# Optimization experiments

Measured on AMD Instinct MI355X. Metric: run time of the kernel, lower is better.

Reference implementation:

```python
import math
from collections import deque
import jax, jax.numpy as jnp
import numpy as np

PS = 16; DF = 256; DS = 16; DLANG = 896; BETA = 2.0
B_SZ = 2; IMG = 512


def setup_inputs():
    key = jax.random.key(0)
    ks = jax.random.split(key, 16)
    def rn(k, shape, scale=1.0):
        return jax.random.normal(k, shape, jnp.float32) * scale
    # W_delta bias init: inverse-softplus of dt ~ LogUniform(1e-3, 1e-1), as in torch _init_weights
    u = jax.random.uniform(ks[15], (DF,), jnp.float32)
    dt = jnp.exp(u * (math.log(0.1) - math.log(0.001)) + math.log(0.001))
    inv_dt = dt + jnp.log(-jnp.expm1(-dt))
    return {
        "images": rn(ks[0], (B_SZ, 3, IMG, IMG)),
        "lang_g": rn(ks[1], (B_SZ, DLANG)),
        "conv1_w": rn(ks[2], (64, 3, 3, 3), 1.0 / math.sqrt(27)),
        "conv1_b": jnp.zeros((64,), jnp.float32),
        "conv2_w": rn(ks[3], (128, 64, 3, 3), 1.0 / math.sqrt(576)),
        "conv2_b": jnp.zeros((128,), jnp.float32),
        "fc_w": rn(ks[4], (DF, 128), 1.0 / math.sqrt(128)),
        "fc_b": jnp.zeros((DF,), jnp.float32),
        "W_gate": rn(ks[5], (DF, DLANG), 1.0 / math.sqrt(DLANG)),
        "W_g_prime": rn(ks[6], (DF, DLANG), 1.0 / math.sqrt(DLANG)),
        "A_log": jnp.log(jnp.broadcast_to(jnp.arange(1, DS + 1, dtype=jnp.float32), (DF, DS))),
        "D": jnp.ones((DF,), jnp.float32),
        "B_w": rn(ks[7], (DS, DF), 1.0 / math.sqrt(DF)),
        "B_b": jnp.zeros((DS,), jnp.float32),
        "C_w": rn(ks[8], (DS, DF), 1.0 / math.sqrt(DF)),
        "C_b": jnp.zeros((DS,), jnp.float32),
        "Wd_w": rn(ks[9], (DF, DF), 1.0 / math.sqrt(DF)),
        "Wd_b": inv_dt,
        "out_w": rn(ks[10], (DF, DF), 1.0 / math.sqrt(DF)),
        "out_b": jnp.zeros((DF,), jnp.float32),
        "ln_g": jnp.ones((DF,), jnp.float32),
        "ln_b": jnp.zeros((DF,), jnp.float32),
    }


def _gelu(x):
    return jax.nn.gelu(x, approximate=False)  # torch nn.GELU() default = exact erf


def _conv(x, w, b):
    y = jax.lax.conv_general_dilated(x, w, (1, 1), 'SAME', dimension_numbers=('NCHW', 'OIHW', 'NCHW'))
    return y + b[None, :, None, None]


def _patch_feats(images, c1w, c1b, c2w, c2b, fcw, fcb):
    B, C, H, W = images.shape
    nH, nW = H // PS, W // PS
    # non-overlapping patchify (== unfold/unfold in torch)
    p = images.reshape(B, C, nH, PS, nW, PS).transpose(0, 2, 4, 1, 3, 5).reshape(B * nH * nW, C, PS, PS)
    h = _gelu(_conv(p, c1w, c1b))
    h = _gelu(_conv(h, c2w, c2b))
    h = h.mean(axis=(2, 3))  # AdaptiveAvgPool2d((1,1))
    feats = (h @ fcw.T + fcb).reshape(B, nH * nW, DF)
    return feats, nH, nW


def _structure(feats, r_sem, nH, nW):
    # Host-side (numpy) Kruskal MST + BFS ordering, mirroring the torch detach().cpu() path.
    f = np.asarray(feats, np.float32)
    r = np.asarray(r_sem, np.float32)
    B, P, _ = f.shape
    src, dst = [], []
    for i in range(nH):
        for j in range(nW):
            u = i * nW + j
            if j + 1 < nW:
                src.append(u); dst.append(u + 1)
            if i + 1 < nH:
                src.append(u); dst.append(u + nW)
    src = np.array(src); dst = np.array(dst)
    bfs_all, par_all = [], []
    for b in range(B):
        fn = f[b] / np.maximum(np.linalg.norm(f[b], axis=1, keepdims=True), 1e-12)
        cos = (fn[src] * fn[dst]).sum(1)
        w = (1.0 - r[b][src]) * (1.0 - r[b][dst]) * (-cos) + 1e-6
        parent = np.arange(P)
        def find(x):
            while parent[x] != x:
                parent[x] = parent[parent[x]]
                x = parent[x]
            return x
        adj = [[] for _ in range(P)]
        cnt = 0
        for idx in np.argsort(w):
            ru, rv = find(int(src[idx])), find(int(dst[idx]))
            if ru != rv:
                parent[ru] = rv
                adj[src[idx]].append(int(dst[idx]))
                adj[dst[idx]].append(int(src[idx]))
                cnt += 1
                if cnt == P - 1:
                    break
        root = int(r[b].argmax())
        vis = [False] * P; par_of = [-1] * P; bfs = []
        q = deque([root]); vis[root] = True
        while q:
            n = q.popleft()
            bfs.append(n)
            for nb in adj[n]:
                if not vis[nb]:
                    vis[nb] = True
                    par_of[nb] = n
                    q.append(nb)
        o2b = [0] * P
        for bi, oi in enumerate(bfs):
            o2b[oi] = bi
        par_bfs = [-1 if par_of[o] == -1 else o2b[par_of[o]] for o in bfs]
        bfs_all.append(bfs); par_all.append(par_bfs)
    return jnp.array(bfs_all, jnp.int32), jnp.array(par_all, jnp.int32)


def _core(feats, r_sem, g_prime, bfs, par, A_log, D, B_w, B_b, C_w, C_b, Wd_w, Wd_b, out_w, out_b, ln_g, ln_b):
    A = -jnp.exp(A_log)  # (DF, DS)
    def one(f_b, r_b, gp, bfs_b, par_b):
        rs = r_b[bfs_b]                                  # (P,)
        X = f_b[bfs_b] + rs[:, None] * gp[None, :]       # (P, DF)
        delta = jax.nn.softplus(X @ Wd_w.T + Wd_b) * (1.0 + BETA * rs[:, None])
        Bp = X @ B_w.T + B_b                             # (P, DS)
        Cp = X @ C_w.T + C_b                             # (P, DS)
        P = X.shape[0]
        def body(H, inp):
            i, d_i, b_i, c_i, x_i, p_i = inp
            A_bar = jnp.exp(d_i[:, None] * A)            # (DF, DS)
            h_par = H[jnp.maximum(p_i, 0)] * (p_i >= 0)  # zeros at root
            h = A_bar * h_par + (d_i[:, None] * b_i[None, :]) * x_i[:, None]
            H = H.at[i].set(h)
            y = (h * c_i[None, :]).sum(-1) + D * x_i
            return H, y
        H0 = jnp.zeros((P, DF, DS), X.dtype)
        _, Y = jax.lax.scan(body, H0, (jnp.arange(P), delta, Bp, Cp, X, par_b))
        Yr = jnp.zeros_like(Y).at[bfs_b].set(Y)          # scatter back to raster order
        o = Yr @ out_w.T + out_b
        mu = o.mean(-1, keepdims=True)
        v = ((o - mu) ** 2).mean(-1, keepdims=True)
        return ln_g * (o - mu) / jnp.sqrt(v + 1e-5) + ln_b
    return jax.vmap(one)(feats, r_sem, g_prime, bfs, par)


def reference(images, lang_g, conv1_w, conv1_b, conv2_w, conv2_b, fc_w, fc_b, W_gate, W_g_prime, A_log, D, B_w, B_b, C_w, C_b, Wd_w, Wd_b, out_w, out_b, ln_g, ln_b):
    feats, nH, nW = _patch_feats(images, conv1_w, conv1_b, conv2_w, conv2_b, fc_w, fc_b)
    g_proj = lang_g @ W_gate.T
    r_sem = jax.nn.sigmoid(jnp.einsum('bd,bpd->bp', g_proj, feats) / math.sqrt(DF))
    bfs, par = _structure(feats, r_sem, nH, nW)
    g_prime = lang_g @ W_g_prime.T
    return _core(feats, r_sem, g_prime, bfs, par, A_log, D, B_w, B_b, C_w, C_b, Wd_w, Wd_b, out_w, out_b, ln_g, ln_b)
```

## Files before the change

kernel.cpp:

```cpp
#include <hip/hip_runtime.h>
#include <cstddef>
#include <cstdint>

#define NB    2
#define NP    1024
#define DFEAT 256
#define DSTATE 16
#define NEDGE 1984

typedef unsigned short ushortb;

typedef float fx16 __attribute__((ext_vector_type(16)));
typedef short s16x8 __attribute__((ext_vector_type(8)));

__device__ __forceinline__ float bf2f(unsigned short u){
  union { unsigned int i; float f; } c; c.i = ((unsigned int)u) << 16; return c.f;
}
__device__ __forceinline__ unsigned short f2bf(float f){
  union { float f; unsigned int i; } c; c.f = f;
  unsigned int u = c.i;
  unsigned int r = (u + 0x7fffu + ((u >> 16) & 1u)) >> 16;
  return (unsigned short)r;
}
__device__ __forceinline__ float ldin(const void* p, size_t i, int isbf){
  return isbf ? bf2f(((const ushortb*)p)[i]) : ((const float*)p)[i];
}
__device__ __forceinline__ float gelu_f(float x){
  return 0.5f * x * (1.0f + erff(x * 0.70710678118654752f));
}
__device__ __forceinline__ unsigned int f2sort(float f){
  union { float f; unsigned int i; } c; c.f = f;
  return (c.i & 0x80000000u) ? ~c.i : (c.i | 0x80000000u);
}

constexpr size_t AL(size_t x){ return (x + 63) & ~(size_t)63; }
constexpr size_t O_W1    = 0;
constexpr size_t O_B1    = AL(O_W1 + 1728);
constexpr size_t O_W2    = AL(O_B1 + 64);
constexpr size_t O_B2    = AL(O_W2 + 73728);
constexpr size_t O_FCW   = AL(O_B2 + 128);
constexpr size_t O_FCB   = AL(O_FCW + 32768);
constexpr size_t O_WDW   = AL(O_FCB + 256);
constexpr size_t O_WDB   = AL(O_WDW + 65536);
constexpr size_t O_BWO   = AL(O_WDB + 256);
constexpr size_t O_BBO   = AL(O_BWO + 4096);
constexpr size_t O_CWO   = AL(O_BBO + 16);
constexpr size_t O_CBO   = AL(O_CWO + 4096);
constexpr size_t O_OW    = AL(O_CBO + 16);
constexpr size_t O_OB    = AL(O_OW + 65536);
constexpr size_t O_AF    = AL(O_OB + 256);
constexpr size_t O_DD    = AL(O_AF + 4096);
constexpr size_t O_LNG   = AL(O_DD + 256);
constexpr size_t O_LNB   = AL(O_LNG + 256);
constexpr size_t O_FEATS = AL(O_LNB + 256);
constexpr size_t O_GPROJ = AL(O_FEATS + (size_t)NB*NP*DFEAT);
constexpr size_t O_GPRIM = AL(O_GPROJ + NB*DFEAT);
constexpr size_t O_RSEM  = AL(O_GPRIM + NB*DFEAT);
constexpr size_t O_BFS   = AL(O_RSEM + NB*NP);
constexpr size_t O_PAR   = AL(O_BFS + NB*NP);
constexpr size_t O_X     = AL(O_PAR + NB*NP);
constexpr size_t O_DELTA = AL(O_X + (size_t)NB*NP*DFEAT);
constexpr size_t O_BP    = AL(O_DELTA + (size_t)NB*NP*DFEAT);
constexpr size_t O_CP    = AL(O_BP + NB*NP*DSTATE);
constexpr size_t O_YR    = AL(O_CP + NB*NP*DSTATE);
constexpr size_t O_FLAG  = AL(O_YR + (size_t)NB*NP*DFEAT);
constexpr size_t O_LVL   = AL(O_FLAG + 64);

__global__ __launch_bounds__(256) void k_sniff(const void* img, float* ws)
{
  __shared__ int cnt;
  int tid = threadIdx.x;
  if (tid == 0) cnt = 0;
  __syncthreads();
  const ushortb* u = (const ushortb*)img;
  int local = 0;
  for (int k = 0; k < 16; k++){
    unsigned short v = u[tid * 16 + k];
    if (v == 0 || v == 0x8000u){ local++; continue; }
    float f = fabsf(bf2f(v));
    if (f >= 1e-8f && f <= 64.f) local++;
  }
  atomicAdd(&cnt, local);
  __syncthreads();
  if (tid == 0) ((int*)(ws + O_FLAG))[0] = (cnt >= 3900) ? 1 : 0;
}

__global__ __launch_bounds__(256) void k_convert(const void* c1w, const void* c1b, const void* c2w,
                          const void* c2b, const void* fcw, const void* fcb,
                          const void* alog, const void* dvec,
                          const void* bw, const void* bb, const void* cw, const void* cb,
                          const void* wdw, const void* wdb,
                          const void* ow, const void* ob,
                          const void* lng, const void* lnb,
                          const void* lang, const void* wgate, const void* wgp,
                          float* ws)
{
  const int F = ((const int*)(ws + O_FLAG))[0];
  if (blockIdx.x >= 3038){
    int row = (blockIdx.x - 3038) * 4 + (threadIdx.x >> 6);
    int lane = threadIdx.x & 63;
    int mat = row >> 9;
    int b   = (row >> 8) & 1;
    int df  = row & 255;
    const void* W = mat ? wgp : wgate;
    float s = 0.f;
    for (int k = lane; k < 896; k += 64)
      s += ldin(lang, (size_t)b * 896 + k, F) * ldin(W, (size_t)df * 896 + k, F);
    s += __shfl_xor(s, 1);  s += __shfl_xor(s, 2);  s += __shfl_xor(s, 4);
    s += __shfl_xor(s, 8);  s += __shfl_xor(s, 16); s += __shfl_xor(s, 32);
    if (lane == 0) ws[(mat ? O_GPRIM : O_GPROJ) + b * 256 + df] = s;
    return;
  }
  if (blockIdx.x >= 990){
    size_t i2 = (size_t)(blockIdx.x - 990) * 256 + threadIdx.x;
    if (i2 < (size_t)NB * NP * DFEAT) ws[O_YR + i2] = 0.f;
    return;
  }
  int i = blockIdx.x * 256 + threadIdx.x;
  if (i < 1728){ ws[O_W1 + i] = ldin(c1w, i, F); return; } i -= 1728;
  if (i < 64){ ws[O_B1 + i] = ldin(c1b, i, F); return; } i -= 64;
  if (i < 73728){
    int s = i >> 11;
    int r = i & 2047;
    int nt = r >> 9;
    int r2 = r & 511;
    int ln = r2 >> 3, e = r2 & 7;
    int oc = nt * 32 + (ln & 31);
    int k  = s * 16 + (ln >> 5) * 8 + e;
    int ic = k & 63, tap = k >> 6;
    float v = ldin(c2w, (size_t)(oc * 64 + ic) * 9 + tap, F);
    ushortb hi = f2bf(v);
    float lo = v - bf2f(hi);
    ushortb* WB = (ushortb*)(ws + O_W2);
    size_t cb = ((size_t)(s * 4 + nt)) * 2;
    WB[cb * 512 + r2]       = hi;
    WB[(cb + 1) * 512 + r2] = f2bf(lo);
    return;
  } i -= 73728;
  if (i < 128){ ws[O_B2 + i] = ldin(c2b, i, F); return; } i -= 128;
  if (i < 32768){ ws[O_FCW + i] = ldin(fcw, i, F); return; } i -= 32768;
  if (i < 256){ ws[O_FCB + i] = ldin(fcb, i, F); return; } i -= 256;
  if (i < 65536){
    int k = i >> 8, df = i & 255;
    ws[O_WDW + i] = ldin(wdw, (size_t)df * 256 + k, F); return;
  } i -= 65536;
  if (i < 256){ ws[O_WDB + i] = ldin(wdb, i, F); return; } i -= 256;
  if (i < 4096){
    int k = i >> 4, s = i & 15;
    ws[O_BWO + i] = ldin(bw, (size_t)s * 256 + k, F); return;
  } i -= 4096;
  if (i < 16){ ws[O_BBO + i] = ldin(bb, i, F); return; } i -= 16;
  if (i < 4096){
    int k = i >> 4, s = i & 15;
    ws[O_CWO + i] = ldin(cw, (size_t)s * 256 + k, F); return;
  } i -= 4096;
  if (i < 16){ ws[O_CBO + i] = ldin(cb, i, F); return; } i -= 16;
  if (i < 65536){
    int k = i >> 8, df = i & 255;
    ws[O_OW + i] = ldin(ow, (size_t)df * 256 + k, F); return;
  } i -= 65536;
  if (i < 256){ ws[O_OB + i] = ldin(ob, i, F); return; } i -= 256;
  if (i < 4096){ ws[O_AF + i] = -expf(ldin(alog, i, F)); return; } i -= 4096;
  if (i < 256){ ws[O_DD + i] = ldin(dvec, i, F); return; } i -= 256;
  if (i < 256){ ws[O_LNG + i] = ldin(lng, i, F); return; } i -= 256;
  if (i < 256){ ws[O_LNB + i] = ldin(lnb, i, F); }
}

__global__ __launch_bounds__(512, 2) void k_patch(const void* __restrict__ img,
                                                  const float* __restrict__ ws,
                                                  float* __restrict__ feats)
{
  __shared__ __align__(16) ushortb Ahi[18 * 18 * 64];
  __shared__ __align__(16) ushortb Alo[18 * 18 * 64];
  __shared__ float timg[768];
  __shared__ float pool4[512];
  __shared__ float pm[128];
  const int F = ((const int*)(ws + O_FLAG))[0];
  const float* W1 = ws + O_W1;  const float* B1 = ws + O_B1;
  const float* FCW = ws + O_FCW; const float* FCB = ws + O_FCB;
  const s16x8* BF = (const s16x8*)(ws + O_W2);

  int blk = blockIdx.x; int b = blk >> 10; int pidx = blk & 1023;
  int ph = pidx >> 5, pw = pidx & 31;
  int tid = threadIdx.x;

  if (tid < 256){
    int y = tid >> 4, x = tid & 15;
    #pragma unroll
    for (int c = 0; c < 3; c++)
      timg[c * 256 + tid] =
        ldin(img, (((size_t)b * 3 + c) * 512 + (ph * 16 + y)) * 512 + (pw * 16 + x), F);
  }
  {
    uint4 z4 = make_uint4(0u, 0u, 0u, 0u);
    for (int r = tid; r < 324; r += 512){
      int y = r / 18, x = r - y * 18;
      if (y == 0 || y == 17 || x == 0 || x == 17){
        #pragma unroll
        for (int m = 0; m < 8; m++){
          *(uint4*)&Ahi[r * 64 + m * 8] = z4;
          *(uint4*)&Alo[r * 64 + m * 8] = z4;
        }
      }
    }
  }
  __syncthreads();

  {
    int p = tid & 255, og = tid >> 8;
    int ii = p >> 4, jj = p & 15;
    float pin[27];
    #pragma unroll
    for (int c = 0; c < 3; c++)
      #pragma unroll
      for (int dy = 0; dy < 3; dy++)
        #pragma unroll
        for (int dx = 0; dx < 3; dx++){
          int y = ii + dy - 1, x = jj + dx - 1;
          bool ok = (y >= 0 && y < 16 && x >= 0 && x < 16);
          pin[c * 9 + dy * 3 + dx] = ok ? timg[c * 256 + y * 16 + x] : 0.f;
        }
    int w1base = __builtin_amdgcn_readfirstlane(og * 32 * 27);
    const float* W1g = W1 + w1base;
    float av[32];
    #pragma unroll
    for (int o = 0; o < 32; o++){
      int oc = og * 32 + o;
      float a = B1[oc];
      #pragma unroll
      for (int t = 0; t < 27; t++) a += W1g[o * 27 + t] * pin[t];
      av[o] = gelu_f(a);
    }
    int r = (ii + 1) * 18 + (jj + 1);
    int sw = (r & 7) << 3;
    #pragma unroll
    for (int m = 0; m < 4; m++){
      unsigned int hp[4], lp[4];
      #pragma unroll
      for (int q = 0; q < 4; q++){
        float v0 = av[m * 8 + 2 * q], v1 = av[m * 8 + 2 * q + 1];
        ushortb h0 = f2bf(v0), h1 = f2bf(v1);
        float l0 = v0 - bf2f(h0), l1 = v1 - bf2f(h1);
        hp[q] = (unsigned int)h0 | ((unsigned int)h1 << 16);
        lp[q] = (unsigned int)f2bf(l0) | ((unsigned int)f2bf(l1) << 16);
      }
      int idx = r * 64 + ((og * 32 + m * 8) ^ sw);
      *(uint4*)&Ahi[idx] = make_uint4(hp[0], hp[1], hp[2], hp[3]);
      *(uint4*)&Alo[idx] = make_uint4(lp[0], lp[1], lp[2], lp[3]);
    }
  }
  __syncthreads();

  int wv = tid >> 6, ln = tid & 63;
  int mg = wv >> 1, ng = wv & 1;
  int l31 = ln & 31, lhi = ln >> 5;
  int xcol = ln & 15, yrow = l31 >> 4;

  fx16 acc[2][2];
  #pragma unroll
  for (int m = 0; m < 2; m++)
    #pragma unroll
    for (int n = 0; n < 2; n++)
      #pragma unroll
      for (int r = 0; r < 16; r++) acc[m][n][r] = 0.f;

#define LDFRAG(S, FA, FB) { \
    int sl = (S); if (sl > 35) sl = 35; \
    int shf = sl >> 2, sub = sl & 3; \
    int dyq = shf / 3, dxq = shf - dyq * 3; \
    int ic0 = sub * 16 + lhi * 8; \
    { int r_ = (mg * 4 + yrow + dyq) * 18 + xcol + dxq; \
      int idx = r_ * 64 + (ic0 ^ ((r_ & 7) << 3)); \
      FA[0][0] = *(const s16x8*)&Ahi[idx]; \
      FA[0][1] = *(const s16x8*)&Alo[idx]; } \
    { int r_ = (mg * 4 + 2 + yrow + dyq) * 18 + xcol + dxq; \
      int idx = r_ * 64 + (ic0 ^ ((r_ & 7) << 3)); \
      FA[1][0] = *(const s16x8*)&Ahi[idx]; \
      FA[1][1] = *(const s16x8*)&Alo[idx]; } \
    { int cb = (sl * 4 + ng * 2) * 2; \
      FB[0][0] = BF[cb * 64 + ln]; \
      FB[0][1] = BF[cb * 64 + 64 + ln]; \
      FB[1][0] = BF[cb * 64 + 128 + ln]; \
      FB[1][1] = BF[cb * 64 + 192 + ln]; } \
  }

#define MSTEP(FA, FB) { \
    acc[0][0] = __builtin_amdgcn_mfma_f32_32x32x16_bf16(FA[0][0], FB[0][0], acc[0][0], 0, 0, 0); \
    acc[0][1] = __builtin_amdgcn_mfma_f32_32x32x16_bf16(FA[0][0], FB[1][0], acc[0][1], 0, 0, 0); \
    acc[1][0] = __builtin_amdgcn_mfma_f32_32x32x16_bf16(FA[1][0], FB[0][0], acc[1][0], 0, 0, 0); \
    acc[1][1] = __builtin_amdgcn_mfma_f32_32x32x16_bf16(FA[1][0], FB[1][0], acc[1][1], 0, 0, 0); \
    acc[0][0] = __builtin_amdgcn_mfma_f32_32x32x16_bf16(FA[0][1], FB[0][0], acc[0][0], 0, 0, 0); \
    acc[0][1] = __builtin_amdgcn_mfma_f32_32x32x16_bf16(FA[0][1], FB[1][0], acc[0][1], 0, 0, 0); \
    acc[1][0] = __builtin_amdgcn_mfma_f32_32x32x16_bf16(FA[1][1], FB[0][0], acc[1][0], 0, 0, 0); \
    acc[1][1] = __builtin_amdgcn_mfma_f32_32x32x16_bf16(FA[1][1], FB[1][0], acc[1][1], 0, 0, 0); \
    acc[0][0] = __builtin_amdgcn_mfma_f32_32x32x16_bf16(FA[0][0], FB[0][1], acc[0][0], 0, 0, 0); \
    acc[0][1] = __builtin_amdgcn_mfma_f32_32x32x16_bf16(FA[0][0], FB[1][1], acc[0][1], 0, 0, 0); \
    acc[1][0] = __builtin_amdgcn_mfma_f32_32x32x16_bf16(FA[1][0], FB[0][1], acc[1][0], 0, 0, 0); \
    acc[1][1] = __builtin_amdgcn_mfma_f32_32x32x16_bf16(FA[1][0], FB[1][1], acc[1][1], 0, 0, 0); \
  }

  {
    s16x8 fa0[2][2], fb0[2][2], fa1[2][2], fb1[2][2];
    LDFRAG(0, fa0, fb0);
    for (int s2 = 0; s2 < 18; s2++){
      LDFRAG(2 * s2 + 1, fa1, fb1);
      MSTEP(fa0, fb0);
      LDFRAG(2 * s2 + 2, fa0, fb0);
      MSTEP(fa1, fb1);
    }
  }
#undef LDFRAG
#undef MSTEP

  #pragma unroll
  for (int n = 0; n < 2; n++){
    int nt = ng * 2 + n;
    float bz = ws[O_B2 + nt * 32 + l31];
    float sum = 0.f;
    #pragma unroll
    for (int m = 0; m < 2; m++)
      #pragma unroll
      for (int r = 0; r < 16; r++)
        sum += gelu_f(acc[m][n][r] + bz);
    sum += __shfl_xor(sum, 32);
    if (lhi == 0) pool4[mg * 128 + nt * 32 + l31] = sum;
  }
  __syncthreads();
  if (tid < 128){
    float sv = pool4[tid] + pool4[128 + tid] + pool4[256 + tid] + pool4[384 + tid];
    pm[tid] = sv * (1.f / 256.f);
  }
  __syncthreads();

  if (tid < 256){
    int df = tid;
    float s = FCB[df];
    const float* wrow = FCW + (size_t)df * 128;
    #pragma unroll
    for (int k = 0; k < 128; k += 4)
      s += wrow[k] * pm[k] + wrow[k + 1] * pm[k + 1]
         + wrow[k + 2] * pm[k + 2] + wrow[k + 3] * pm[k + 3];
    feats[((size_t)(b * 1024 + pidx)) * 256 + df] = s;
  }
}

__device__ __forceinline__ void edge_uv(int e, int& u, int& v){
  if (e < 1953){
    int i = e / 63; int k = e - i * 63;
    if (k < 62){ int j = k >> 1; u = i * 32 + j; v = (k & 1) ? u + 32 : u + 1; }
    else { u = i * 32 + 31; v = u + 32; }
  } else { u = 31 * 32 + (e - 1953); v = u + 1; }
}

__global__ __launch_bounds__(1024) void k_struct(float* __restrict__ ws)
{
  __shared__ float s_ninv[1024];
  __shared__ float s_w[NEDGE];
  __shared__ float s_r[1024];
  __shared__ int   s_comp[1024];
  __shared__ int   s_link[1024];
  __shared__ int   s_link2[1024];
  __shared__ unsigned long long s_best[1024];
  __shared__ unsigned char  s_mst[NEDGE];
  __shared__ unsigned short s_adj[1024 * 4];
  __shared__ unsigned char  s_deg[1024];
  __shared__ unsigned short s_bfs[1024];
  __shared__ short          s_parof[1024];
  __shared__ unsigned short s_o2b[1024];
  __shared__ unsigned short s_cur[1024];
  __shared__ unsigned short s_nxt[1024];
  __shared__ unsigned short s_off[1025];
  __shared__ unsigned short s_loff2[1026];
  __shared__ unsigned long long s_rootkey;
  __shared__ int s_ncomp, s_cursz, s_bfscnt, s_nextsz, s_nlvl;

  int b = blockIdx.x; int tid = threadIdx.x;
  const float* feats = ws + O_FEATS + (size_t)b * NP * DFEAT;

  {
    const float4* f4 = (const float4*)(feats + (size_t)tid * 256);
    const float4* g4 = (const float4*)(ws + O_GPROJ + b * 256);
    float d = 0.f, gdot = 0.f;
    for (int k = 0; k < 64; k++){
      float4 q = f4[k]; float4 g = g4[k];
      d += q.x*q.x + q.y*q.y + q.z*q.z + q.w*q.w;
      gdot += q.x*g.x + q.y*g.y + q.z*g.z + q.w*g.w;
    }
    s_ninv[tid] = 1.f / fmaxf(sqrtf(d), 1e-12f);
    float r = 1.f / (1.f + expf(-gdot * (1.f / 16.f)));
    s_r[tid] = r;
    ws[O_RSEM + b * NP + tid] = r;
    s_comp[tid] = tid;
    s_deg[tid] = 0;
    s_bfs[tid] = (unsigned short)tid;
    s_o2b[tid] = (unsigned short)tid;
    s_parof[tid] = -1;
  }
  for (int e = tid; e < NEDGE; e += 1024) s_mst[e] = 0;
  __syncthreads();

  for (int e = tid; e < NEDGE; e += 1024){
    int u, v; edge_uv(e, u, v);
    const float4* fu = (const float4*)(feats + (size_t)u * 256);
    const float4* fv = (const float4*)(feats + (size_t)v * 256);
    float d = 0.f;
    for (int k = 0; k < 64; k++){ float4 a = fu[k], c = fv[k]; d += a.x*c.x + a.y*c.y + a.z*c.z + a.w*c.w; }
    float cosv = d * s_ninv[u] * s_ninv[v];
    s_w[e] = (1.f - s_r[u]) * (1.f - s_r[v]) * (-cosv) + 1e-6f;
  }
  __syncthreads();

  for (int round = 0; round < 12; round++){
    s_best[tid] = ~0ull;
    __syncthreads();
    for (int e = tid; e < NEDGE; e += 1024){
      int u, v; edge_uv(e, u, v);
      int cu = s_comp[u], cv = s_comp[v];
      if (cu != cv){
        unsigned long long key = (((unsigned long long)f2sort(s_w[e])) << 32) | (unsigned int)e;
        atomicMin(&s_best[cu], key);
        atomicMin(&s_best[cv], key);
      }
    }
    __syncthreads();
    int l = tid;
    if (s_comp[tid] == tid && s_best[tid] != ~0ull){
      int e = (int)(s_best[tid] & 0xffffffffu);
      int u, v; edge_uv(e, u, v);
      s_mst[e] = 1;
      int cu = s_comp[u], cv = s_comp[v];
      l = (cu == tid) ? cv : cu;
    }
    s_link[tid] = l;
    __syncthreads();
    if (l != tid && s_link[l] == tid && tid < l) s_link[tid] = tid;
    __syncthreads();
    for (int it = 0; it < 10; it++){
      int x = s_link[tid]; s_link2[tid] = s_link[x];
      __syncthreads();
      s_link[tid] = s_link2[tid];
      __syncthreads();
    }
    s_comp[tid] = s_link[s_comp[tid]];
    if (tid == 0) s_ncomp = 0;
    __syncthreads();
    if (s_comp[tid] == tid) atomicAdd(&s_ncomp, 1);
    __syncthreads();
    if (s_ncomp == 1) break;
    __syncthreads();
  }
  __syncthreads();

  {
    int v = tid; int i = v >> 5, j = v & 31;
    float wloc[4]; int nloc[4]; int d = 0;
    if (j > 0){ int e = (i < 31) ? (i * 63 + 2 * (j - 1)) : (1953 + (j - 1));
      if (s_mst[e]){ wloc[d] = s_w[e]; nloc[d] = v - 1; d++; } }
    if (j < 31){ int e = (i < 31) ? (i * 63 + 2 * j) : (1953 + j);
      if (s_mst[e]){ wloc[d] = s_w[e]; nloc[d] = v + 1; d++; } }
    if (i > 0){ int e = (i - 1) * 63 + ((j < 31) ? (2 * j + 1) : 62);
      if (s_mst[e]){ wloc[d] = s_w[e]; nloc[d] = v - 32; d++; } }
    if (i < 31){ int e = i * 63 + ((j < 31) ? (2 * j + 1) : 62);
      if (s_mst[e]){ wloc[d] = s_w[e]; nloc[d] = v + 32; d++; } }
    for (int a = 1; a < d; a++){
      float wv = wloc[a]; int nv = nloc[a]; int c = a - 1;
      while (c >= 0 && wloc[c] > wv){ wloc[c+1] = wloc[c]; nloc[c+1] = nloc[c]; c--; }
      wloc[c+1] = wv; nloc[c+1] = nv;
    }
    s_deg[v] = (unsigned char)d;
    for (int a = 0; a < d; a++) s_adj[v * 4 + a] = (unsigned short)nloc[a];
  }
  if (tid == 0) s_rootkey = 0ull;
  __syncthreads();
  {
    unsigned long long key = (((unsigned long long)f2sort(s_r[tid])) << 32) | (unsigned int)(1023 - tid);
    atomicMax(&s_rootkey, key);
  }
  __syncthreads();
  int root = 1023 - (int)(s_rootkey & 0xffffffffu);

  if (tid == 0){
    s_bfs[0] = (unsigned short)root; s_o2b[root] = 0; s_parof[root] = -1;
    s_cur[0] = (unsigned short)root; s_cursz = 1; s_bfscnt = 1; s_nlvl = 0;
  }
  __syncthreads();
  for (int lev = 0; lev < 1024; lev++){
    int csz = s_cursz;
    if (csz <= 0) break;
    if (tid < 64){
      int runbase = 0;
      for (int t0 = 0; t0 < csz; t0 += 64){
        int t = t0 + tid;
        int cnt = 0;
        if (t < csz){
          int n = s_cur[t];
          cnt = (int)s_deg[n] - (s_parof[n] >= 0 ? 1 : 0);
        }
        int v = cnt;
        #pragma unroll
        for (int off = 1; off < 64; off <<= 1){
          int u2 = __shfl_up(v, off);
          if (tid >= off) v += u2;
        }
        if (t < csz) s_off[t] = (unsigned short)(runbase + v - cnt);
        runbase += __shfl(v, 63);
      }
      if (tid == 0){
        if (s_nlvl < 1025){ s_loff2[s_nlvl] = (unsigned short)(s_bfscnt - csz); }
        s_nlvl++;
        s_nextsz = runbase;
      }
    }
    __syncthreads();
    if (tid < csz){
      int n = s_cur[tid]; int base = s_off[tid]; int k = 0;
      int pn = s_parof[n]; int dg = s_deg[n];
      for (int a = 0; a < dg; a++){
        int c = s_adj[n * 4 + a];
        if (c == pn) continue;
        s_parof[c] = (short)n;
        if (base + k < 1024) s_nxt[base + k] = (unsigned short)c;
        int pos = s_bfscnt + base + k;
        if (pos < 1024){
          s_bfs[pos] = (unsigned short)c;
          s_o2b[c] = (unsigned short)pos;
        }
        k++;
      }
    }
    __syncthreads();
    if (tid == 0){ s_bfscnt += s_nextsz; s_cursz = (s_nextsz > 1024) ? 1024 : s_nextsz; }
    __syncthreads();
    if (tid < s_cursz) s_cur[tid] = s_nxt[tid];
    __syncthreads();
  }
  __syncthreads();

  int* BFSo = (int*)(ws + O_BFS);
  int* PARo = (int*)(ws + O_PAR);
  {
    int node = s_bfs[tid] & 1023;
    BFSo[b * 1024 + tid] = node;
    int p = s_parof[node];
    PARo[b * 1024 + tid] = (p < 0) ? -1 : (int)(s_o2b[p] & 1023);
  }
  {
    int* LVLo = (int*)(ws + O_LVL) + b * 1040;
    int nl = s_nlvl; if (nl > 1024) nl = 1024;
    if (tid == 0){ LVLo[0] = nl; LVLo[1 + nl] = NP; }
    if (tid < nl) LVLo[1 + tid] = (int)s_loff2[tid];
  }
}

__global__ __launch_bounds__(256) void k_xdelta(float* __restrict__ ws)
{
  __shared__ float xs[256];
  int blk = blockIdx.x; int b = blk >> 10, i = blk & 1023; int df = threadIdx.x;
  const int* BFSo = (const int*)(ws + O_BFS);
  int node = BFSo[b * 1024 + i] & 1023;
  float rs = ws[O_RSEM + b * 1024 + node];
  float xv = ws[O_FEATS + ((size_t)(b * 1024 + node)) * 256 + df] + rs * ws[O_GPRIM + b * 256 + df];
  xs[df] = xv;
  ws[O_X + ((size_t)(b * 1024 + i)) * 256 + df] = xv;
  __syncthreads();
  {
    const float* WT = ws + O_WDW;
    float z = ws[O_WDB + df];
    #pragma unroll 8
    for (int k = 0; k < 256; k++)
      z += WT[(size_t)k * 256 + df] * xs[k];
    float sp = fmaxf(z, 0.f) + log1pf(expf(-fabsf(z)));
    ws[O_DELTA + ((size_t)(b * 1024 + i)) * 256 + df] = sp * (1.f + 2.f * rs);
  }
  if (df < 32){
    int s = df & 15;
    const float* WT = ws + ((df < 16) ? O_BWO : O_CWO);
    float a = ws[((df < 16) ? O_BBO : O_CBO) + s];
    #pragma unroll 8
    for (int k = 0; k < 256; k++) a += WT[k * 16 + s] * xs[k];
    ws[((df < 16) ? O_BP : O_CP) + (size_t)(b * 1024 + i) * 16 + s] = a;
  }
}

__global__ __launch_bounds__(256) void k_scan(float* __restrict__ ws)
{
  __shared__ float h[NP * DSTATE];
  __shared__ float xs[NP];
  __shared__ float ds[NP];
  __shared__ int   par_s[NP];
  __shared__ int   bfs_s[NP];
  int blk = blockIdx.x; int b = blk >> 8, f = blk & 255;
  int tid = threadIdx.x;
  int g = tid >> 4, s = tid & 15;
  const int* PARo = (const int*)(ws + O_PAR);
  const int* BFSo = (const int*)(ws + O_BFS);
  const int* LVLo = (const int*)(ws + O_LVL) + b * 1040;
  for (int i = tid; i < NP; i += 256){
    xs[i] = ws[O_X     + ((size_t)(b * NP + i)) * DFEAT + f];
    ds[i] = ws[O_DELTA + ((size_t)(b * NP + i)) * DFEAT + f];
    par_s[i] = PARo[b * NP + i];
    bfs_s[i] = BFSo[b * NP + i] & 1023;
  }
  __syncthreads();

  int nlvl = LVLo[0];
  bool degen = (nlvl < 1 || nlvl > NP);
  if (degen) nlvl = NP;

  float Aln = ws[O_AF + f * 16 + s];
  float Dv  = ws[O_DD + f];
  const float* Bp = ws + O_BP + (size_t)b * NP * DSTATE;
  const float* Cp = ws + O_CP + (size_t)b * NP * DSTATE;
  float* Yr = ws + O_YR + (size_t)b * NP * DFEAT;

  for (int l = 0; l < nlvl; l++){
    int o0, o1;
    if (degen){ o0 = l; o1 = l + 1; }
    else {
      o0 = LVLo[1 + l]; o1 = LVLo[2 + l];
      o0 = (o0 < 0) ? 0 : ((o0 > NP) ? NP : o0);
      o1 = (o1 < o0) ? o0 : ((o1 > NP) ? NP : o1);
    }
    for (int i = o0 + g; i < o1; i += 16){
      int p = par_s[i];
      float d = ds[i], x = xs[i];
      float hp = (p >= 0 && p < i) ? h[p * 16 + s] : 0.f;
      float hn = expf(d * Aln) * hp + d * Bp[i * 16 + s] * x;
      h[i * 16 + s] = hn;
      float t = hn * Cp[i * 16 + s];
      t += __shfl_xor(t, 1); t += __shfl_xor(t, 2);
      t += __shfl_xor(t, 4); t += __shfl_xor(t, 8);
      if (s == 0) Yr[(size_t)bfs_s[i] * DFEAT + f] = t + Dv * x;
    }
    __syncthreads();
  }
}

__global__ __launch_bounds__(256) void k_outln(const float* __restrict__ ws,
                                               void* __restrict__ out)
{
  __shared__ float yl[256];
  __shared__ float red[8];
  const int F = ((const int*)(ws + O_FLAG))[0];
  int blk = blockIdx.x; int b = blk >> 10, p = blk & 1023; int df = threadIdx.x;
  yl[df] = ws[O_YR + ((size_t)(b * 1024 + p)) * 256 + df];
  __syncthreads();
  const float* OT = ws + O_OW;
  float a = ws[O_OB + df];
  #pragma unroll 8
  for (int k = 0; k < 256; k++)
    a += OT[(size_t)k * 256 + df] * yl[k];
  int lane = df & 63, wid = df >> 6;
  float t = a;
  t += __shfl_xor(t, 1); t += __shfl_xor(t, 2);  t += __shfl_xor(t, 4);
  t += __shfl_xor(t, 8); t += __shfl_xor(t, 16); t += __shfl_xor(t, 32);
  if (lane == 0) red[wid] = t;
  __syncthreads();
  float mu = (red[0] + red[1] + red[2] + red[3]) * (1.f / 256.f);
  float dv = a - mu;
  float t2 = dv * dv;
  t2 += __shfl_xor(t2, 1); t2 += __shfl_xor(t2, 2);  t2 += __shfl_xor(t2, 4);
  t2 += __shfl_xor(t2, 8); t2 += __shfl_xor(t2, 16); t2 += __shfl_xor(t2, 32);
  if (lane == 0) red[4 + wid] = t2;
  __syncthreads();
  float var = (red[4] + red[5] + red[6] + red[7]) * (1.f / 256.f);
  float o = ws[O_LNG + df] * dv / sqrtf(var + 1e-5f) + ws[O_LNB + df];
  size_t idx = ((size_t)(b * 1024 + p)) * 256 + df;
  if (F) ((ushortb*)out)[idx] = f2bf(o);
  else   ((float*)out)[idx]   = o;
}

extern "C" void kernel_launch(void* const* d_in, const int* in_sizes, int n_in,
                              void* d_out, int out_size, void* d_ws, size_t ws_size,
                              hipStream_t stream)
{
  (void)in_sizes; (void)n_in; (void)out_size; (void)ws_size;
  const void* img   = d_in[0];
  const void* lang  = d_in[1];
  const void* c1w   = d_in[2];
  const void* c1b   = d_in[3];
  const void* c2w   = d_in[4];
  const void* c2b   = d_in[5];
  const void* fcw   = d_in[6];
  const void* fcb   = d_in[7];
  const void* wgate = d_in[8];
  const void* wgp   = d_in[9];
  const void* alog  = d_in[10];
  const void* dvec  = d_in[11];
  const void* bw    = d_in[12];
  const void* bb    = d_in[13];
  const void* cw    = d_in[14];
  const void* cb    = d_in[15];
  const void* wdw   = d_in[16];
  const void* wdb   = d_in[17];
  const void* ow    = d_in[18];
  const void* ob    = d_in[19];
  const void* lng   = d_in[20];
  const void* lnb   = d_in[21];
  float* ws = (float*)d_ws;

  k_sniff<<<1, 256, 0, stream>>>(img, ws);
  k_convert<<<990 + 2048 + 256, 256, 0, stream>>>(c1w, c1b, c2w, c2b, fcw, fcb, alog, dvec,
                                                  bw, bb, cw, cb, wdw, wdb, ow, ob, lng, lnb,
                                                  lang, wgate, wgp, ws);
  k_patch<<<2048, 512, 0, stream>>>(img, ws, ws + O_FEATS);
  k_struct<<<2, 1024, 0, stream>>>(ws);
  k_xdelta<<<2048, 256, 0, stream>>>(ws);
  k_scan<<<NB * DFEAT, 256, 0, stream>>>(ws);
  k_outln<<<2048, 256, 0, stream>>>(ws, d_out);
}
```

Before: 881.0 us.

## Split conv2 input channels into two halves to shrink LDS and raise occupancy

The conv1 output staged in LDS is now split into two 32-channel halves. Each half is computed, stored in bf16 hi/lo form and consumed by the MFMA conv2 loop in turn, so the LDS tiles are half as large and launch bounds ask for 4 blocks per CU instead of 2. The conv2 weight prepack is reordered to match the chunked K order, and the LDS swizzle is adjusted for the 32-channel row. Separately, the Boruvka pointer-jumping loop with a fixed 10 iterations and barriers is replaced by a per-thread walk to the root. The costs are an extra barrier pair per chunk, conv1 input gathers done twice, and tighter register limits that may cause spills.

```diff
diff --git a/kernel.cpp b/kernel.cpp
--- a/kernel.cpp
+++ b/kernel.cpp
@@ -120,19 +120,20 @@
   if (i < 1728){ ws[O_W1 + i] = ldin(c1w, i, F); return; } i -= 1728;
   if (i < 64){ ws[O_B1 + i] = ldin(c1b, i, F); return; } i -= 64;
   if (i < 73728){
-    int s = i >> 11;
+    int sg = i >> 11;
     int r = i & 2047;
     int nt = r >> 9;
     int r2 = r & 511;
     int ln = r2 >> 3, e = r2 & 7;
+    int c  = sg / 18, s = sg - c * 18;
+    int tap = s >> 1, ksub = s & 1;
     int oc = nt * 32 + (ln & 31);
-    int k  = s * 16 + (ln >> 5) * 8 + e;
-    int ic = k & 63, tap = k >> 6;
+    int ic = c * 32 + ksub * 16 + (ln >> 5) * 8 + e;
     float v = ldin(c2w, (size_t)(oc * 64 + ic) * 9 + tap, F);
     ushortb hi = f2bf(v);
     float lo = v - bf2f(hi);
     ushortb* WB = (ushortb*)(ws + O_W2);
-    size_t cb = ((size_t)(s * 4 + nt)) * 2;
+    size_t cb = ((size_t)(sg * 4 + nt)) * 2;
     WB[cb * 512 + r2]       = hi;
     WB[(cb + 1) * 512 + r2] = f2bf(lo);
     return;
@@ -166,12 +167,12 @@
   if (i < 256){ ws[O_LNB + i] = ldin(lnb, i, F); }
 }
 
-__global__ __launch_bounds__(512, 2) void k_patch(const void* __restrict__ img,
+__global__ __launch_bounds__(512, 4) void k_patch(const void* __restrict__ img,
                                                   const float* __restrict__ ws,
                                                   float* __restrict__ feats)
 {
-  __shared__ __align__(16) ushortb Ahi[18 * 18 * 64];
-  __shared__ __align__(16) ushortb Alo[18 * 18 * 64];
+  __shared__ __align__(16) ushortb Ahi[18 * 18 * 32];
+  __shared__ __align__(16) ushortb Alo[18 * 18 * 32];
   __shared__ float timg[768];
   __shared__ float pool4[512];
   __shared__ float pm[128];
@@ -197,56 +198,11 @@
       int y = r / 18, x = r - y * 18;
       if (y == 0 || y == 17 || x == 0 || x == 17){
         #pragma unroll
-        for (int m = 0; m < 8; m++){
-          *(uint4*)&Ahi[r * 64 + m * 8] = z4;
-          *(uint4*)&Alo[r * 64 + m * 8] = z4;
+        for (int m = 0; m < 4; m++){
+          *(uint4*)&Ahi[r * 32 + m * 8] = z4;
+          *(uint4*)&Alo[r * 32 + m * 8] = z4;
         }
       }
-    }
-  }
-  __syncthreads();
-
-  {
-    int p = tid & 255, og = tid >> 8;
-    int ii = p >> 4, jj = p & 15;
-    float pin[27];
-    #pragma unroll
-    for (int c = 0; c < 3; c++)
-      #pragma unroll
-      for (int dy = 0; dy < 3; dy++)
-        #pragma unroll
-        for (int dx = 0; dx < 3; dx++){
-          int y = ii + dy - 1, x = jj + dx - 1;
-          bool ok = (y >= 0 && y < 16 && x >= 0 && x < 16);
-          pin[c * 9 + dy * 3 + dx] = ok ? timg[c * 256 + y * 16 + x] : 0.f;
-        }
-    int w1base = __builtin_amdgcn_readfirstlane(og * 32 * 27);
-    const float* W1g = W1 + w1base;
-    float av[32];
-    #pragma unroll
-    for (int o = 0; o < 32; o++){
-      int oc = og * 32 + o;
-      float a = B1[oc];
-      #pragma unroll
-      for (int t = 0; t < 27; t++) a += W1g[o * 27 + t] * pin[t];
-      av[o] = gelu_f(a);
-    }
-    int r = (ii + 1) * 18 + (jj + 1);
-    int sw = (r & 7) << 3;
-    #pragma unroll
-    for (int m = 0; m < 4; m++){
-      unsigned int hp[4], lp[4];
-      #pragma unroll
-      for (int q = 0; q < 4; q++){
-        float v0 = av[m * 8 + 2 * q], v1 = av[m * 8 + 2 * q + 1];
-        ushortb h0 = f2bf(v0), h1 = f2bf(v1);
-        float l0 = v0 - bf2f(h0), l1 = v1 - bf2f(h1);
-        hp[q] = (unsigned int)h0 | ((unsigned int)h1 << 16);
-        lp[q] = (unsigned int)f2bf(l0) | ((unsigned int)f2bf(l1) << 16);
-      }
-      int idx = r * 64 + ((og * 32 + m * 8) ^ sw);
-      *(uint4*)&Ahi[idx] = make_uint4(hp[0], hp[1], hp[2], hp[3]);
-      *(uint4*)&Alo[idx] = make_uint4(lp[0], lp[1], lp[2], lp[3]);
     }
   }
   __syncthreads();
@@ -255,6 +211,8 @@
   int mg = wv >> 1, ng = wv & 1;
   int l31 = ln & 31, lhi = ln >> 5;
   int xcol = ln & 15, yrow = l31 >> 4;
+  int p = tid & 255, og = tid >> 8;
+  int ii = p >> 4, jj = p & 15;
 
   fx16 acc[2][2];
   #pragma unroll
@@ -265,19 +223,19 @@
       for (int r = 0; r < 16; r++) acc[m][n][r] = 0.f;
 
 #define LDFRAG(S, FA, FB) { \
-    int sl = (S); if (sl > 35) sl = 35; \
-    int shf = sl >> 2, sub = sl & 3; \
-    int dyq = shf / 3, dxq = shf - dyq * 3; \
-    int ic0 = sub * 16 + lhi * 8; \
+    int sl = (S); if (sl > 17) sl = 17; \
+    int tap = sl >> 1, ksub = sl & 1; \
+    int dyq = tap / 3, dxq = tap - dyq * 3; \
+    int icq0 = ksub * 2 + lhi; \
     { int r_ = (mg * 4 + yrow + dyq) * 18 + xcol + dxq; \
-      int idx = r_ * 64 + (ic0 ^ ((r_ & 7) << 3)); \
+      int idx = r_ * 32 + ((icq0 ^ ((r_ >> 1) & 3)) << 3); \
       FA[0][0] = *(const s16x8*)&Ahi[idx]; \
       FA[0][1] = *(const s16x8*)&Alo[idx]; } \
     { int r_ = (mg * 4 + 2 + yrow + dyq) * 18 + xcol + dxq; \
-      int idx = r_ * 64 + (ic0 ^ ((r_ & 7) << 3)); \
+      int idx = r_ * 32 + ((icq0 ^ ((r_ >> 1) & 3)) << 3); \
       FA[1][0] = *(const s16x8*)&Ahi[idx]; \
       FA[1][1] = *(const s16x8*)&Alo[idx]; } \
-    { int cb = (sl * 4 + ng * 2) * 2; \
+    { int cb = ((cbase + sl) * 4 + ng * 2) * 2; \
       FB[0][0] = BF[cb * 64 + ln]; \
       FB[0][1] = BF[cb * 64 + 64 + ln]; \
       FB[1][0] = BF[cb * 64 + 128 + ln]; \
@@ -299,15 +257,62 @@
     acc[1][1] = __builtin_amdgcn_mfma_f32_32x32x16_bf16(FA[1][0], FB[1][1], acc[1][1], 0, 0, 0); \
   }
 
-  {
-    s16x8 fa0[2][2], fb0[2][2], fa1[2][2], fb1[2][2];
-    LDFRAG(0, fa0, fb0);
-    for (int s2 = 0; s2 < 18; s2++){
-      LDFRAG(2 * s2 + 1, fa1, fb1);
-      MSTEP(fa0, fb0);
-      LDFRAG(2 * s2 + 2, fa0, fb0);
-      MSTEP(fa1, fb1);
-    }
+  for (int c = 0; c < 2; c++){
+    {
+      float pin[27];
+      #pragma unroll
+      for (int cc = 0; cc < 3; cc++)
+        #pragma unroll
+        for (int dy = 0; dy < 3; dy++)
+          #pragma unroll
+          for (int dx = 0; dx < 3; dx++){
+            int y = ii + dy - 1, x = jj + dx - 1;
+            bool ok = (y >= 0 && y < 16 && x >= 0 && x < 16);
+            pin[cc * 9 + dy * 3 + dx] = ok ? timg[cc * 256 + y * 16 + x] : 0.f;
+          }
+      int oc0 = c * 32 + og * 16;
+      int w1base = __builtin_amdgcn_readfirstlane(oc0 * 27);
+      const float* W1g = W1 + w1base;
+      float av[16];
+      #pragma unroll
+      for (int o = 0; o < 16; o++){
+        float a = B1[oc0 + o];
+        #pragma unroll
+        for (int t = 0; t < 27; t++) a += W1g[o * 27 + t] * pin[t];
+        av[o] = gelu_f(a);
+      }
+      int r = (ii + 1) * 18 + (jj + 1);
+      int swz = ((r >> 1) & 3) << 3;
+      #pragma unroll
+      for (int g = 0; g < 2; g++){
+        unsigned int hp[4], lp[4];
+        #pragma unroll
+        for (int q = 0; q < 4; q++){
+          float v0 = av[g * 8 + 2 * q], v1 = av[g * 8 + 2 * q + 1];
+          ushortb h0 = f2bf(v0), h1 = f2bf(v1);
+          float l0 = v0 - bf2f(h0), l1 = v1 - bf2f(h1);
+          hp[q] = (unsigned int)h0 | ((unsigned int)h1 << 16);
+          lp[q] = (unsigned int)f2bf(l0) | ((unsigned int)f2bf(l1) << 16);
+        }
+        int idx = r * 32 + (((og * 2 + g) << 3) ^ swz);
+        *(uint4*)&Ahi[idx] = make_uint4(hp[0], hp[1], hp[2], hp[3]);
+        *(uint4*)&Alo[idx] = make_uint4(lp[0], lp[1], lp[2], lp[3]);
+      }
+    }
+    __syncthreads();
+
+    {
+      int cbase = c * 18;
+      s16x8 fa0[2][2], fb0[2][2], fa1[2][2], fb1[2][2];
+      LDFRAG(0, fa0, fb0);
+      for (int s2 = 0; s2 < 9; s2++){
+        LDFRAG(2 * s2 + 1, fa1, fb1);
+        MSTEP(fa0, fb0);
+        LDFRAG(2 * s2 + 2, fa0, fb0);
+        MSTEP(fa1, fb1);
+      }
+    }
+    __syncthreads();
   }
 #undef LDFRAG
 #undef MSTEP
@@ -435,13 +440,14 @@
     __syncthreads();
     if (l != tid && s_link[l] == tid && tid < l) s_link[tid] = tid;
     __syncthreads();
-    for (int it = 0; it < 10; it++){
-      int x = s_link[tid]; s_link2[tid] = s_link[x];
-      __syncthreads();
-      s_link[tid] = s_link2[tid];
-      __syncthreads();
-    }
-    s_comp[tid] = s_link[s_comp[tid]];
+    {
+      int x = tid;
+      int p = s_link[x];
+      while (p != x){ x = p; p = s_link[x]; }
+      s_link2[tid] = x;
+    }
+    __syncthreads();
+    s_comp[tid] = s_link2[s_comp[tid]];
     if (tid == 0) s_ncomp = 0;
     __syncthreads();
     if (s_comp[tid] == tid) atomicAdd(&s_ncomp, 1);
```

Result: slower. 1.315 ms (+49.3%).
